# Kernel tuning notes

Measured on AMD Instinct MI355X. Metric: run time of the kernel, lower is better.

Reference implementation:

```python
import math
import jax, jax.numpy as jnp
import numpy as np

L, W, H, T, B = 12, 1024, 16, 1024, 2
CH = W // H  # per-head channels
SCALE = 1.0 / math.sqrt(math.sqrt(CH))
STD = 0.25 * math.sqrt(1.0 / W)  # init_scale * sqrt(1/width)


def setup_inputs() -> dict:
    key = jax.random.key(0)
    ks = jax.random.split(key, 8)
    x = jax.random.normal(ks[0], (B, T, W), dtype=jnp.float32)
    qkv_w = jax.random.normal(ks[1], (L, W, 3 * W), dtype=jnp.float32) * STD
    qkv_b = jnp.zeros((L, 3 * W), jnp.float32)
    proj_w = jax.random.normal(ks[2], (L, W, W), dtype=jnp.float32) * STD
    proj_b = jnp.zeros((L, W), jnp.float32)
    ln1_g = jnp.ones((L, W), jnp.float32)
    ln1_b = jnp.zeros((L, W), jnp.float32)
    ln2_g = jnp.ones((L, W), jnp.float32)
    ln2_b = jnp.zeros((L, W), jnp.float32)
    fc_w = jax.random.normal(ks[3], (L, W, 4 * W), dtype=jnp.float32) * STD
    fc_b = jnp.zeros((L, 4 * W), jnp.float32)
    fc2_w = jax.random.normal(ks[4], (L, 4 * W, W), dtype=jnp.float32) * STD
    fc2_b = jnp.zeros((L, W), jnp.float32)
    return dict(x=x, qkv_w=qkv_w, qkv_b=qkv_b, proj_w=proj_w, proj_b=proj_b,
                ln1_g=ln1_g, ln1_b=ln1_b, ln2_g=ln2_g, ln2_b=ln2_b,
                fc_w=fc_w, fc_b=fc_b, fc2_w=fc2_w, fc2_b=fc2_b)


def _ln(x, g, b, eps=1e-5):
    mu = jnp.mean(x, axis=-1, keepdims=True)
    var = jnp.mean(jnp.square(x - mu), axis=-1, keepdims=True)
    return (x - mu) * jax.lax.rsqrt(var + eps) * g + b


def _attn(h, w_qkv, b_qkv, w_p, b_p):
    bs, t, w = h.shape
    qkv = (h @ w_qkv + b_qkv).reshape(bs, t, H, 3 * CH)
    q, k, v = jnp.split(qkv, 3, axis=-1)  # each [bs, t, H, CH]
    # double-sqrt scaling as in QKVMultiheadAttention
    wts = jnp.einsum('bthc,bshc->bhts', q * SCALE, k * SCALE)
    wts = jax.nn.softmax(wts.astype(jnp.float32), axis=-1).astype(h.dtype)
    o = jnp.einsum('bhts,bshc->bthc', wts, v).reshape(bs, t, w)
    return o @ w_p + b_p


def reference(x, qkv_w, qkv_b, proj_w, proj_b, ln1_g, ln1_b, ln2_g, ln2_b,
              fc_w, fc_b, fc2_w, fc2_b):
    def step(h, p):
        wq, bq, wp, bp, g1, b1, g2, b2, wf, bf, w2, b2m = p
        h = h + _attn(_ln(h, g1, b1), wq, bq, wp, bp)
        z = _ln(h, g2, b2)
        h = h + (jax.nn.gelu(z @ wf + bf, approximate=False) @ w2 + b2m)
        return h, None
    params = (qkv_w, qkv_b, proj_w, proj_b, ln1_g, ln1_b, ln2_g, ln2_b,
              fc_w, fc_b, fc2_w, fc2_b)
    out, _ = jax.lax.scan(step, x, params)
    return out
```

## Files before the change

kernel.cpp:

```cpp
#include <hip/hip_runtime.h>
#include <hip/hip_bf16.h>
#include <math.h>

typedef __bf16 bf16;
typedef __bf16 bf16x8 __attribute__((ext_vector_type(8)));
typedef __bf16 bf16x4 __attribute__((ext_vector_type(4)));
typedef float  f32x4  __attribute__((ext_vector_type(4)));

#define DEV __device__ __forceinline__

DEV void lds_load16(const void* g, void* l) {
  __builtin_amdgcn_global_load_lds(
      (__attribute__((address_space(1))) unsigned int*)g,
      (__attribute__((address_space(3))) unsigned int*)l, 16, 0, 0);
}

DEV f32x4 mfma16(bf16x8 a, bf16x8 b, f32x4 c) {
  return __builtin_amdgcn_mfma_f32_16x16x32_bf16(a, b, c, 0, 0, 0);
}

__global__ void copy_f32(const float* __restrict__ in, float* __restrict__ out) {
  int i = blockIdx.x * blockDim.x + threadIdx.x;
  ((float4*)out)[i] = ((const float4*)in)[i];
}

__global__ __launch_bounds__(256) void transpose_cvt(
    const float* __restrict__ in0, bf16* __restrict__ out0, int R, int C) {
  __shared__ float t[32][33];
  size_t zo = (size_t)blockIdx.z * R * C;
  const float* in = in0 + zo;
  bf16* out = out0 + zo;
  int tx = threadIdx.x, ty = threadIdx.y;
  int c0 = blockIdx.x * 32, r0 = blockIdx.y * 32;
#pragma unroll
  for (int i = 0; i < 4; i++)
    t[ty + i * 8][tx] = in[(size_t)(r0 + ty + i * 8) * C + c0 + tx];
  __syncthreads();
#pragma unroll
  for (int i = 0; i < 4; i++)
    out[(size_t)(c0 + ty + i * 8) * R + r0 + tx] = (bf16)t[tx][ty + i * 8];
}

__global__ __launch_bounds__(256) void ln_fwd(
    const float* __restrict__ x, const float* __restrict__ gw,
    const float* __restrict__ bw, bf16* __restrict__ y) {
  int row = blockIdx.x, tid = threadIdx.x;
  const float4 v = ((const float4*)(x + (size_t)row * 1024))[tid];
  float s  = v.x + v.y + v.z + v.w;
  float s2 = v.x * v.x + v.y * v.y + v.z * v.z + v.w * v.w;
#pragma unroll
  for (int o = 1; o < 64; o <<= 1) {
    s  += __shfl_xor(s, o);
    s2 += __shfl_xor(s2, o);
  }
  __shared__ float ps[4], ps2[4];
  int wv = tid >> 6;
  if ((tid & 63) == 0) { ps[wv] = s; ps2[wv] = s2; }
  __syncthreads();
  s  = ps[0] + ps[1] + ps[2] + ps[3];
  s2 = ps2[0] + ps2[1] + ps2[2] + ps2[3];
  float mu  = s * (1.f / 1024.f);
  float var = s2 * (1.f / 1024.f) - mu * mu;
  float rs  = rsqrtf(var + 1e-5f);
  float4 gv = ((const float4*)gw)[tid];
  float4 bv = ((const float4*)bw)[tid];
  bf16x4 o4;
  o4[0] = (bf16)((v.x - mu) * rs * gv.x + bv.x);
  o4[1] = (bf16)((v.y - mu) * rs * gv.y + bv.y);
  o4[2] = (bf16)((v.z - mu) * rs * gv.z + bv.z);
  o4[3] = (bf16)((v.w - mu) * rs * gv.w + bv.w);
  *(bf16x4*)(y + (size_t)row * 1024 + tid * 4) = o4;
}

__global__ __launch_bounds__(256) void reduce_ln(
    const float* __restrict__ parts, int nparts, const float* __restrict__ bias,
    float* __restrict__ h, const float* __restrict__ gw,
    const float* __restrict__ bw, bf16* __restrict__ y) {
  const int row = blockIdx.x, tid = threadIdx.x;
  const size_t MN = (size_t)gridDim.x * 1024;
  const size_t rb = (size_t)row * 256;
  float4 s = ((const float4*)parts)[rb + tid];
  for (int p = 1; p < nparts; p++) {
    float4 v = ((const float4*)(parts + (size_t)p * MN))[rb + tid];
    s.x += v.x; s.y += v.y; s.z += v.z; s.w += v.w;
  }
  const float4 bb = ((const float4*)bias)[tid];
  float4 r = ((float4*)h)[rb + tid];
  r.x += s.x + bb.x; r.y += s.y + bb.y; r.z += s.z + bb.z; r.w += s.w + bb.w;
  ((float4*)h)[rb + tid] = r;
  if (gw == nullptr) return;
  float sm  = r.x + r.y + r.z + r.w;
  float sm2 = r.x * r.x + r.y * r.y + r.z * r.z + r.w * r.w;
#pragma unroll
  for (int o = 1; o < 64; o <<= 1) {
    sm  += __shfl_xor(sm, o);
    sm2 += __shfl_xor(sm2, o);
  }
  __shared__ float ps[4], ps2[4];
  int wv = tid >> 6;
  if ((tid & 63) == 0) { ps[wv] = sm; ps2[wv] = sm2; }
  __syncthreads();
  sm  = ps[0] + ps[1] + ps[2] + ps[3];
  sm2 = ps2[0] + ps2[1] + ps2[2] + ps2[3];
  float mu  = sm * (1.f / 1024.f);
  float var = sm2 * (1.f / 1024.f) - mu * mu;
  float rs  = rsqrtf(var + 1e-5f);
  float4 gv = ((const float4*)gw)[tid];
  float4 bv = ((const float4*)bw)[tid];
  bf16x4 o4;
  o4[0] = (bf16)((r.x - mu) * rs * gv.x + bv.x);
  o4[1] = (bf16)((r.y - mu) * rs * gv.y + bv.y);
  o4[2] = (bf16)((r.z - mu) * rs * gv.z + bv.z);
  o4[3] = (bf16)((r.w - mu) * rs * gv.w + bv.w);
  *(bf16x4*)(y + (size_t)row * 1024 + tid * 4) = o4;
}

template <int EPI>
__global__ __launch_bounds__(512, 2) void gemm8p(
    const bf16* __restrict__ A, const bf16* __restrict__ Bt,
    const float* __restrict__ bias, float* __restrict__ outf,
    bf16* __restrict__ outb, int M, int N, int K, int kcount) {
  __shared__ __align__(16) char lds[3 * 49152];
  const int tid = threadIdx.x, wv = tid >> 6, lane = tid & 63;
  const int g = lane >> 4, lr = lane & 15;
  const int wr = wv >> 2, wc = wv & 3;
  const int bn = blockIdx.x, bm = blockIdx.y;
  const int kbegin = blockIdx.z * kcount;
  const bf16* Ab = A + (size_t)bm * 128 * K + kbegin;
  const bf16* Bb = Bt + (size_t)bn * 256 * K + kbegin;
  const int nt = kcount >> 6;

  f32x4 acc[4][4] = {};

  auto stageA = [&](int t) {
    char* dst = lds + (t % 3) * 49152;
    int k0 = t * 64;
#pragma unroll
    for (int c = 0; c < 2; c++) {
      int off = c * 8192 + tid * 16;
      int row = off >> 7, cb = off & 127;
      int cbs = cb ^ ((row & 7) << 4);
      lds_load16((const char*)(Ab + (size_t)row * K + k0) + cbs, dst + off);
    }
  };
  auto stageB = [&](int t, int half) {
    char* dst = lds + (t % 3) * 49152 + 16384 + half * 16384;
    int k0 = t * 64;
#pragma unroll
    for (int c = 0; c < 2; c++) {
      int off = c * 8192 + tid * 16;
      int row = (off >> 7) + half * 128, cb = off & 127;
      int cbs = cb ^ ((row & 7) << 4);
      lds_load16((const char*)(Bb + (size_t)row * K + k0) + cbs, dst + off);
    }
  };
  auto ldA = [&](int t, int m, int kk) -> bf16x8 {
    const char* base = lds + (t % 3) * 49152;
    int row = wr * 64 + m * 16 + lr;
    int col = (kk * 64 + g * 16) ^ ((row & 7) << 4);
    return *(const bf16x8*)(base + row * 128 + col);
  };
  auto ldB = [&](int t, int n, int kk) -> bf16x8 {
    const char* base = lds + (t % 3) * 49152 + 16384;
    int row = wc * 64 + n * 16 + lr;
    int col = (kk * 64 + g * 16) ^ ((row & 7) << 4);
    return *(const bf16x8*)(base + row * 128 + col);
  };

  stageA(0); stageB(0, 0); stageB(0, 1);
  if (nt > 1) {
    stageA(1); stageB(1, 0); stageB(1, 1);
    asm volatile("s_waitcnt vmcnt(6)" ::: "memory");
  } else {
    asm volatile("s_waitcnt vmcnt(0)" ::: "memory");
  }
  __builtin_amdgcn_s_barrier();

  bf16x8 a[4][2], b[4][2];
  for (int t = 0; t < nt; ++t) {
#pragma unroll
    for (int m = 0; m < 4; m++)
#pragma unroll
      for (int kk = 0; kk < 2; kk++) a[m][kk] = ldA(t, m, kk);
#pragma unroll
    for (int n = 0; n < 2; n++)
#pragma unroll
      for (int kk = 0; kk < 2; kk++) b[n][kk] = ldB(t, n, kk);
    if (t + 2 < nt) { stageA(t + 2); stageB(t + 2, 0); }
    __builtin_amdgcn_s_barrier();
    asm volatile("s_waitcnt lgkmcnt(0)" ::: "memory");
    __builtin_amdgcn_sched_barrier(0);
    __builtin_amdgcn_s_setprio(1);
#pragma unroll
    for (int m = 0; m < 4; m++)
#pragma unroll
      for (int n = 0; n < 2; n++)
#pragma unroll
        for (int kk = 0; kk < 2; kk++)
          acc[m][n] = mfma16(a[m][kk], b[n][kk], acc[m][n]);
    __builtin_amdgcn_s_setprio(0);
    __builtin_amdgcn_s_barrier();
#pragma unroll
    for (int n = 2; n < 4; n++)
#pragma unroll
      for (int kk = 0; kk < 2; kk++) b[n][kk] = ldB(t, n, kk);
    if (t + 2 < nt) {
      stageB(t + 2, 1);
      asm volatile("s_waitcnt vmcnt(6)" ::: "memory");
    } else if (t + 1 < nt) {
      asm volatile("s_waitcnt vmcnt(0)" ::: "memory");
    }
    __builtin_amdgcn_s_barrier();
    asm volatile("s_waitcnt lgkmcnt(0)" ::: "memory");
    __builtin_amdgcn_sched_barrier(0);
    __builtin_amdgcn_s_setprio(1);
#pragma unroll
    for (int m = 0; m < 4; m++)
#pragma unroll
      for (int n = 2; n < 4; n++)
#pragma unroll
        for (int kk = 0; kk < 2; kk++)
          acc[m][n] = mfma16(a[m][kk], b[n][kk], acc[m][n]);
    __builtin_amdgcn_s_setprio(0);
    __builtin_amdgcn_s_barrier();
  }

  float* po = (EPI == 3) ? outf + (size_t)blockIdx.z * M * N : outf;
#pragma unroll
  for (int m = 0; m < 4; m++) {
#pragma unroll
    for (int n = 0; n < 4; n++) {
      int col = bn * 256 + wc * 64 + n * 16 + lr;
      float bv = (EPI == 3) ? 0.f : bias[col];
#pragma unroll
      for (int r = 0; r < 4; r++) {
        int row = bm * 128 + wr * 64 + m * 16 + g * 4 + r;
        size_t idx = (size_t)row * N + col;
        float v = acc[m][n][r] + bv;
        if (EPI == 0) {
          outb[idx] = (bf16)v;
        } else if (EPI == 2) {
          outb[idx] = (bf16)(0.5f * v * (1.f + erff(v * 0.70710678118f)));
        } else {
          po[idx] = v;
        }
      }
    }
  }
}

__global__ __launch_bounds__(256) void attn_fwd(
    const bf16* __restrict__ qkv, bf16* __restrict__ outp) {
  __shared__ __align__(16) bf16 Kls[128 * 64];
  __shared__ __align__(16) bf16 Vt[64 * 128];
  __shared__ __align__(16) bf16 Pls[4 * 32 * 128];
  const int tid = threadIdx.x, wv = tid >> 6, lane = tid & 63;
  const int g = lane >> 4, lr = lane & 15;
  const int bh = blockIdx.y, bb = bh >> 4, hh = bh & 15;
  const int q0 = blockIdx.x * 128;
  const bf16* base = qkv + (size_t)bb * 1024 * 3072;
  const int qc = hh * 192, kc = qc + 64, vc = qc + 128;

  bf16x8 aq[2][2];
#pragma unroll
  for (int m = 0; m < 2; m++)
#pragma unroll
    for (int kk = 0; kk < 2; kk++) {
      int row = q0 + wv * 32 + m * 16 + lr;
      aq[m][kk] = *(const bf16x8*)(base + (size_t)row * 3072 + qc + kk * 32 + g * 8);
    }

  f32x4 o[2][4] = {};
  float rm[2][4], rl[2][4];
#pragma unroll
  for (int m = 0; m < 2; m++)
#pragma unroll
    for (int r = 0; r < 4; r++) { rm[m][r] = -1e30f; rl[m][r] = 0.f; }

  for (int s0 = 0; s0 < 1024; s0 += 128) {
#pragma unroll
    for (int c = 0; c < 4; c++) {
      int off = wv * 4096 + c * 1024 + lane * 16;
      int s = off >> 7, cb = off & 127;
      int cbs = cb ^ ((s & 7) << 4);
      lds_load16((const char*)(base + (size_t)(s0 + s) * 3072 + kc) + cbs,
                 (char*)Kls + off);
    }
#pragma unroll
    for (int it = 0; it < 4; it++) {
      int idx = it * 256 + tid;
      int s = idx >> 3, c0i = (idx & 7) * 8;
      bf16x8 vvv = *(const bf16x8*)(base + (size_t)(s0 + s) * 3072 + vc + c0i);
#pragma unroll
      for (int j = 0; j < 8; j++) {
        int c = c0i + j;
        *(bf16*)((char*)Vt + c * 256 + ((s * 2) ^ ((c & 7) << 4))) = vvv[j];
      }
    }
    __syncthreads();
    f32x4 sa[2][8] = {};
#pragma unroll
    for (int kk = 0; kk < 2; kk++) {
#pragma unroll
      for (int n = 0; n < 8; n++) {
        int srow = n * 16 + lr;
        int cbyte = (kk * 32 + g * 8) * 2;
        bf16x8 kb = *(const bf16x8*)((char*)Kls + srow * 128 +
                                     (cbyte ^ ((srow & 7) << 4)));
        sa[0][n] = mfma16(aq[0][kk], kb, sa[0][n]);
        sa[1][n] = mfma16(aq[1][kk], kb, sa[1][n]);
      }
    }
#pragma unroll
    for (int m = 0; m < 2; m++) {
      float al[4];
#pragma unroll
      for (int r = 0; r < 4; r++) {
        float tm = -1e30f;
#pragma unroll
        for (int n = 0; n < 8; n++) {
          sa[m][n][r] *= 0.125f;
          tm = fmaxf(tm, sa[m][n][r]);
        }
        tm = fmaxf(tm, __shfl_xor(tm, 1));
        tm = fmaxf(tm, __shfl_xor(tm, 2));
        tm = fmaxf(tm, __shfl_xor(tm, 4));
        tm = fmaxf(tm, __shfl_xor(tm, 8));
        float nm = fmaxf(rm[m][r], tm);
        al[r] = __expf(rm[m][r] - nm);
        rm[m][r] = nm;
      }
      float psum[4] = {0.f, 0.f, 0.f, 0.f};
#pragma unroll
      for (int n = 0; n < 8; n++) {
#pragma unroll
        for (int r = 0; r < 4; r++) {
          float p = __expf(sa[m][n][r] - rm[m][r]);
          psum[r] += p;
          int rw = m * 16 + g * 4 + r;
          int sb = (n * 16 + lr) * 2;
          *(bf16*)((char*)Pls + wv * 8192 + rw * 256 + (sb ^ ((rw & 7) << 4))) =
              (bf16)p;
        }
      }
#pragma unroll
      for (int r = 0; r < 4; r++) {
        psum[r] += __shfl_xor(psum[r], 1);
        psum[r] += __shfl_xor(psum[r], 2);
        psum[r] += __shfl_xor(psum[r], 4);
        psum[r] += __shfl_xor(psum[r], 8);
        rl[m][r] = rl[m][r] * al[r] + psum[r];
#pragma unroll
        for (int n = 0; n < 4; n++) o[m][n][r] *= al[r];
      }
    }
    __syncthreads();
#pragma unroll
    for (int sc = 0; sc < 4; sc++) {
      bf16x8 pa[2];
#pragma unroll
      for (int m = 0; m < 2; m++) {
        int rw = m * 16 + lr;
        int sb = (sc * 32 + g * 8) * 2;
        pa[m] = *(const bf16x8*)((char*)Pls + wv * 8192 + rw * 256 +
                                 (sb ^ ((rw & 7) << 4)));
      }
#pragma unroll
      for (int n = 0; n < 4; n++) {
        int c = n * 16 + lr;
        int sb = (sc * 32 + g * 8) * 2;
        bf16x8 vb = *(const bf16x8*)((char*)Vt + c * 256 + (sb ^ ((c & 7) << 4)));
        o[0][n] = mfma16(pa[0], vb, o[0][n]);
        o[1][n] = mfma16(pa[1], vb, o[1][n]);
      }
    }
    __syncthreads();
  }
#pragma unroll
  for (int m = 0; m < 2; m++)
#pragma unroll
    for (int n = 0; n < 4; n++)
#pragma unroll
      for (int r = 0; r < 4; r++) {
        int row = q0 + wv * 32 + m * 16 + g * 4 + r;
        int col = hh * 64 + n * 16 + lr;
        outp[(size_t)(bb * 1024 + row) * 1024 + col] =
            (bf16)(o[m][n][r] / rl[m][r]);
      }
}

extern "C" void kernel_launch(void* const* d_in, const int* in_sizes, int n_in,
                              void* d_out, int out_size, void* d_ws,
                              size_t ws_size, hipStream_t stream) {
  const float* x      = (const float*)d_in[0];
  const float* qkv_w  = (const float*)d_in[1];
  const float* qkv_b  = (const float*)d_in[2];
  const float* proj_w = (const float*)d_in[3];
  const float* proj_b = (const float*)d_in[4];
  const float* ln1_g  = (const float*)d_in[5];
  const float* ln1_b  = (const float*)d_in[6];
  const float* ln2_g  = (const float*)d_in[7];
  const float* ln2_b  = (const float*)d_in[8];
  const float* fc_w   = (const float*)d_in[9];
  const float* fc_b   = (const float*)d_in[10];
  const float* fc2_w  = (const float*)d_in[11];
  const float* fc2_b  = (const float*)d_in[12];
  float* h = (float*)d_out;

  char* ws = (char*)d_ws;
  size_t off = 0;
  auto alloc = [&](size_t bytes) -> char* {
    char* p = ws + off;
    off = (off + bytes + 255) & ~(size_t)255;
    return p;
  };
  bf16* wq_t    = (bf16*)alloc((size_t)12 * 3072 * 1024 * 2);
  bf16* wp_t    = (bf16*)alloc((size_t)12 * 1024 * 1024 * 2);
  bf16* wf_t    = (bf16*)alloc((size_t)12 * 4096 * 1024 * 2);
  bf16* w2_t    = (bf16*)alloc((size_t)12 * 1024 * 4096 * 2);
  bf16* lnbuf   = (bf16*)alloc((size_t)2048 * 1024 * 2);
  bf16* qkvbuf  = (bf16*)alloc((size_t)2048 * 3072 * 2);
  bf16* attnbuf = (bf16*)alloc((size_t)2048 * 1024 * 2);
  bf16* fcbuf   = (bf16*)alloc((size_t)2048 * 4096 * 2);
  float* partbuf = (float*)alloc((size_t)4 * 2048 * 1024 * 4);

  transpose_cvt<<<dim3(96, 32, 12), dim3(32, 8), 0, stream>>>(qkv_w, wq_t, 1024, 3072);
  transpose_cvt<<<dim3(32, 32, 12), dim3(32, 8), 0, stream>>>(proj_w, wp_t, 1024, 1024);
  transpose_cvt<<<dim3(128, 32, 12), dim3(32, 8), 0, stream>>>(fc_w, wf_t, 1024, 4096);
  transpose_cvt<<<dim3(32, 128, 12), dim3(32, 8), 0, stream>>>(fc2_w, w2_t, 4096, 1024);

  copy_f32<<<2048, 256, 0, stream>>>(x, h);
  ln_fwd<<<2048, 256, 0, stream>>>(h, ln1_g, ln1_b, lnbuf);

  for (int l = 0; l < 12; l++) {
    const bf16* wq = wq_t + (size_t)l * 3072 * 1024;
    const bf16* wp = wp_t + (size_t)l * 1024 * 1024;
    const bf16* wf = wf_t + (size_t)l * 4096 * 1024;
    const bf16* w2 = w2_t + (size_t)l * 1024 * 4096;

    gemm8p<0><<<dim3(12, 16, 1), 512, 0, stream>>>(
        lnbuf, wq, qkv_b + (size_t)l * 3072, nullptr, qkvbuf, 2048, 3072, 1024,
        1024);
    attn_fwd<<<dim3(8, 32), 256, 0, stream>>>(qkvbuf, attnbuf);
    gemm8p<3><<<dim3(4, 16, 2), 512, 0, stream>>>(
        attnbuf, wp, nullptr, partbuf, nullptr, 2048, 1024, 1024, 512);
    reduce_ln<<<2048, 256, 0, stream>>>(partbuf, 2, proj_b + (size_t)l * 1024,
                                        h, ln2_g + (size_t)l * 1024,
                                        ln2_b + (size_t)l * 1024, lnbuf);
    gemm8p<2><<<dim3(16, 16, 1), 512, 0, stream>>>(
        lnbuf, wf, fc_b + (size_t)l * 4096, nullptr, fcbuf, 2048, 4096, 1024,
        1024);
    gemm8p<3><<<dim3(4, 16, 4), 512, 0, stream>>>(
        fcbuf, w2, nullptr, partbuf, nullptr, 2048, 1024, 4096, 1024);
    if (l < 11) {
      reduce_ln<<<2048, 256, 0, stream>>>(
          partbuf, 4, fc2_b + (size_t)l * 1024, h,
          ln1_g + (size_t)(l + 1) * 1024, ln1_b + (size_t)(l + 1) * 1024,
          lnbuf);
    } else {
      reduce_ln<<<2048, 256, 0, stream>>>(partbuf, 4,
                                          fc2_b + (size_t)l * 1024, h, nullptr,
                                          nullptr, nullptr);
    }
  }
}
```

Measured before the change: 2.035 ms.

## Load GEMM A operand straight to registers, stage only B in LDS

The GEMM now reads the A tile directly from global memory into registers for each k-step and uses LDS only for the B tile. This frees LDS, allowing a 128-wide N tile for the projection and FC2 GEMMs. FC2 split-K drops from 4 to 2, which halves the partial buffer and the reduce traffic. The initial copy kernel is folded into the first layernorm. The direct A loads lose LDS reuse across the four column waves, so more global/L2 traffic is exchanged for lower LDS pressure and fewer barriers.

```diff
diff --git a/kernel.cpp b/kernel.cpp
--- a/kernel.cpp
+++ b/kernel.cpp
@@ -17,11 +17,6 @@
 
 DEV f32x4 mfma16(bf16x8 a, bf16x8 b, f32x4 c) {
   return __builtin_amdgcn_mfma_f32_16x16x32_bf16(a, b, c, 0, 0, 0);
-}
-
-__global__ void copy_f32(const float* __restrict__ in, float* __restrict__ out) {
-  int i = blockIdx.x * blockDim.x + threadIdx.x;
-  ((float4*)out)[i] = ((const float4*)in)[i];
 }
 
 __global__ __launch_bounds__(256) void transpose_cvt(
@@ -43,9 +38,11 @@
 
 __global__ __launch_bounds__(256) void ln_fwd(
     const float* __restrict__ x, const float* __restrict__ gw,
-    const float* __restrict__ bw, bf16* __restrict__ y) {
+    const float* __restrict__ bw, bf16* __restrict__ y,
+    float* __restrict__ hout) {
   int row = blockIdx.x, tid = threadIdx.x;
   const float4 v = ((const float4*)(x + (size_t)row * 1024))[tid];
+  if (hout) ((float4*)(hout + (size_t)row * 1024))[tid] = v;
   float s  = v.x + v.y + v.z + v.w;
   float s2 = v.x * v.x + v.y * v.y + v.z * v.z + v.w * v.w;
 #pragma unroll
@@ -115,122 +112,128 @@
   *(bf16x4*)(y + (size_t)row * 1024 + tid * 4) = o4;
 }
 
-template <int EPI>
-__global__ __launch_bounds__(512, 2) void gemm8p(
+template <int BN, int EPI>
+__global__ __launch_bounds__(512, 2) void gemm_ad(
     const bf16* __restrict__ A, const bf16* __restrict__ Bt,
     const float* __restrict__ bias, float* __restrict__ outf,
     bf16* __restrict__ outb, int M, int N, int K, int kcount) {
-  __shared__ __align__(16) char lds[3 * 49152];
+  constexpr int NF = BN / 64;
+  constexpr int SLOT = BN * 64 * 2;
+  constexpr int NCH = BN / 64;
+  __shared__ __align__(16) char lds[3 * SLOT];
   const int tid = threadIdx.x, wv = tid >> 6, lane = tid & 63;
   const int g = lane >> 4, lr = lane & 15;
   const int wr = wv >> 2, wc = wv & 3;
   const int bn = blockIdx.x, bm = blockIdx.y;
   const int kbegin = blockIdx.z * kcount;
-  const bf16* Ab = A + (size_t)bm * 128 * K + kbegin;
-  const bf16* Bb = Bt + (size_t)bn * 256 * K + kbegin;
+  const bf16* Ab =
+      A + (size_t)(bm * 128 + wr * 64 + lr) * K + kbegin + g * 8;
+  const bf16* Bb = Bt + (size_t)bn * BN * K + kbegin;
   const int nt = kcount >> 6;
-
-  f32x4 acc[4][4] = {};
-
-  auto stageA = [&](int t) {
-    char* dst = lds + (t % 3) * 49152;
-    int k0 = t * 64;
-#pragma unroll
-    for (int c = 0; c < 2; c++) {
-      int off = c * 8192 + tid * 16;
-      int row = off >> 7, cb = off & 127;
-      int cbs = cb ^ ((row & 7) << 4);
-      lds_load16((const char*)(Ab + (size_t)row * K + k0) + cbs, dst + off);
-    }
+  f32x4 acc[4][NF] = {};
+
+  auto stageC = [&](int t, int c) {
+    char* dst = lds + (t % 3) * SLOT;
+    int off = c * 8192 + tid * 16;
+    int row = off >> 7, cb = off & 127;
+    lds_load16((const char*)(Bb + (size_t)row * K + t * 64) +
+                   (cb ^ ((row & 7) << 4)),
+               dst + off);
   };
-  auto stageB = [&](int t, int half) {
-    char* dst = lds + (t % 3) * 49152 + 16384 + half * 16384;
-    int k0 = t * 64;
-#pragma unroll
-    for (int c = 0; c < 2; c++) {
-      int off = c * 8192 + tid * 16;
-      int row = (off >> 7) + half * 128, cb = off & 127;
-      int cbs = cb ^ ((row & 7) << 4);
-      lds_load16((const char*)(Bb + (size_t)row * K + k0) + cbs, dst + off);
-    }
-  };
-  auto ldA = [&](int t, int m, int kk) -> bf16x8 {
-    const char* base = lds + (t % 3) * 49152;
-    int row = wr * 64 + m * 16 + lr;
+  auto ldB = [&](int t, int n, int kk) -> bf16x8 {
+    const char* base = lds + (t % 3) * SLOT;
+    int row = wc * (BN / 4) + n * 16 + lr;
     int col = (kk * 64 + g * 16) ^ ((row & 7) << 4);
     return *(const bf16x8*)(base + row * 128 + col);
   };
-  auto ldB = [&](int t, int n, int kk) -> bf16x8 {
-    const char* base = lds + (t % 3) * 49152 + 16384;
-    int row = wc * 64 + n * 16 + lr;
-    int col = (kk * 64 + g * 16) ^ ((row & 7) << 4);
-    return *(const bf16x8*)(base + row * 128 + col);
-  };
-
-  stageA(0); stageB(0, 0); stageB(0, 1);
-  if (nt > 1) {
-    stageA(1); stageB(1, 0); stageB(1, 1);
-    asm volatile("s_waitcnt vmcnt(6)" ::: "memory");
-  } else {
-    asm volatile("s_waitcnt vmcnt(0)" ::: "memory");
-  }
+
+  for (int c = 0; c < NCH; c++) stageC(0, c);
+  if (nt > 1)
+    for (int c = 0; c < NCH; c++) stageC(1, c);
+  if (NCH == 4)
+    asm volatile("s_waitcnt vmcnt(4)" ::: "memory");
+  else
+    asm volatile("s_waitcnt vmcnt(2)" ::: "memory");
   __builtin_amdgcn_s_barrier();
 
-  bf16x8 a[4][2], b[4][2];
   for (int t = 0; t < nt; ++t) {
+    bf16x8 a[4][2];
 #pragma unroll
     for (int m = 0; m < 4; m++)
 #pragma unroll
-      for (int kk = 0; kk < 2; kk++) a[m][kk] = ldA(t, m, kk);
-#pragma unroll
-    for (int n = 0; n < 2; n++)
-#pragma unroll
-      for (int kk = 0; kk < 2; kk++) b[n][kk] = ldB(t, n, kk);
-    if (t + 2 < nt) { stageA(t + 2); stageB(t + 2, 0); }
-    __builtin_amdgcn_s_barrier();
-    asm volatile("s_waitcnt lgkmcnt(0)" ::: "memory");
-    __builtin_amdgcn_sched_barrier(0);
-    __builtin_amdgcn_s_setprio(1);
-#pragma unroll
-    for (int m = 0; m < 4; m++)
+      for (int kk = 0; kk < 2; kk++)
+        a[m][kk] =
+            *(const bf16x8*)(Ab + (size_t)m * 16 * K + t * 64 + kk * 32);
+
+    if constexpr (BN == 256) {
+      bf16x8 b[2][2];
 #pragma unroll
       for (int n = 0; n < 2; n++)
 #pragma unroll
-        for (int kk = 0; kk < 2; kk++)
-          acc[m][n] = mfma16(a[m][kk], b[n][kk], acc[m][n]);
-    __builtin_amdgcn_s_setprio(0);
-    __builtin_amdgcn_s_barrier();
-#pragma unroll
-    for (int n = 2; n < 4; n++)
-#pragma unroll
-      for (int kk = 0; kk < 2; kk++) b[n][kk] = ldB(t, n, kk);
-    if (t + 2 < nt) {
-      stageB(t + 2, 1);
-      asm volatile("s_waitcnt vmcnt(6)" ::: "memory");
-    } else if (t + 1 < nt) {
-      asm volatile("s_waitcnt vmcnt(0)" ::: "memory");
-    }
-    __builtin_amdgcn_s_barrier();
-    asm volatile("s_waitcnt lgkmcnt(0)" ::: "memory");
-    __builtin_amdgcn_sched_barrier(0);
-    __builtin_amdgcn_s_setprio(1);
-#pragma unroll
-    for (int m = 0; m < 4; m++)
-#pragma unroll
-      for (int n = 2; n < 4; n++)
-#pragma unroll
-        for (int kk = 0; kk < 2; kk++)
-          acc[m][n] = mfma16(a[m][kk], b[n][kk], acc[m][n]);
-    __builtin_amdgcn_s_setprio(0);
-    __builtin_amdgcn_s_barrier();
+        for (int kk = 0; kk < 2; kk++) b[n][kk] = ldB(t, n, kk);
+      if (t + 2 < nt) { stageC(t + 2, 0); stageC(t + 2, 1); }
+      __builtin_amdgcn_s_barrier();
+      asm volatile("s_waitcnt lgkmcnt(0)" ::: "memory");
+      __builtin_amdgcn_sched_barrier(0);
+      __builtin_amdgcn_s_setprio(1);
+#pragma unroll
+      for (int m = 0; m < 4; m++)
+#pragma unroll
+        for (int n = 0; n < 2; n++)
+#pragma unroll
+          for (int kk = 0; kk < 2; kk++)
+            acc[m][n] = mfma16(a[m][kk], b[n][kk], acc[m][n]);
+      __builtin_amdgcn_s_setprio(0);
+      __builtin_amdgcn_s_barrier();
+#pragma unroll
+      for (int n = 0; n < 2; n++)
+#pragma unroll
+        for (int kk = 0; kk < 2; kk++) b[n][kk] = ldB(t, n + 2, kk);
+      if (t + 2 < nt) { stageC(t + 2, 2); stageC(t + 2, 3); }
+      asm volatile("s_waitcnt vmcnt(4)" ::: "memory");
+      __builtin_amdgcn_s_barrier();
+      asm volatile("s_waitcnt lgkmcnt(0)" ::: "memory");
+      __builtin_amdgcn_sched_barrier(0);
+      __builtin_amdgcn_s_setprio(1);
+#pragma unroll
+      for (int m = 0; m < 4; m++)
+#pragma unroll
+        for (int n = 0; n < 2; n++)
+#pragma unroll
+          for (int kk = 0; kk < 2; kk++)
+            acc[m][n + 2] = mfma16(a[m][kk], b[n][kk], acc[m][n + 2]);
+      __builtin_amdgcn_s_setprio(0);
+      __builtin_amdgcn_s_barrier();
+    } else {
+      bf16x8 b[NF][2];
+#pragma unroll
+      for (int n = 0; n < NF; n++)
+#pragma unroll
+        for (int kk = 0; kk < 2; kk++) b[n][kk] = ldB(t, n, kk);
+      if (t + 2 < nt) { stageC(t + 2, 0); stageC(t + 2, 1); }
+      asm volatile("s_waitcnt vmcnt(2)" ::: "memory");
+      __builtin_amdgcn_s_barrier();
+      asm volatile("s_waitcnt lgkmcnt(0)" ::: "memory");
+      __builtin_amdgcn_sched_barrier(0);
+      __builtin_amdgcn_s_setprio(1);
+#pragma unroll
+      for (int m = 0; m < 4; m++)
+#pragma unroll
+        for (int n = 0; n < NF; n++)
+#pragma unroll
+          for (int kk = 0; kk < 2; kk++)
+            acc[m][n] = mfma16(a[m][kk], b[n][kk], acc[m][n]);
+      __builtin_amdgcn_s_setprio(0);
+      __builtin_amdgcn_s_barrier();
+    }
   }
 
   float* po = (EPI == 3) ? outf + (size_t)blockIdx.z * M * N : outf;
 #pragma unroll
   for (int m = 0; m < 4; m++) {
 #pragma unroll
-    for (int n = 0; n < 4; n++) {
-      int col = bn * 256 + wc * 64 + n * 16 + lr;
+    for (int n = 0; n < NF; n++) {
+      int col = bn * BN + wc * (BN / 4) + n * 16 + lr;
       float bv = (EPI == 3) ? 0.f : bias[col];
 #pragma unroll
       for (int r = 0; r < 4; r++) {
@@ -422,15 +425,14 @@
   bf16* qkvbuf  = (bf16*)alloc((size_t)2048 * 3072 * 2);
   bf16* attnbuf = (bf16*)alloc((size_t)2048 * 1024 * 2);
   bf16* fcbuf   = (bf16*)alloc((size_t)2048 * 4096 * 2);
-  float* partbuf = (float*)alloc((size_t)4 * 2048 * 1024 * 4);
+  float* partbuf = (float*)alloc((size_t)2 * 2048 * 1024 * 4);
 
   transpose_cvt<<<dim3(96, 32, 12), dim3(32, 8), 0, stream>>>(qkv_w, wq_t, 1024, 3072);
   transpose_cvt<<<dim3(32, 32, 12), dim3(32, 8), 0, stream>>>(proj_w, wp_t, 1024, 1024);
   transpose_cvt<<<dim3(128, 32, 12), dim3(32, 8), 0, stream>>>(fc_w, wf_t, 1024, 4096);
   transpose_cvt<<<dim3(32, 128, 12), dim3(32, 8), 0, stream>>>(fc2_w, w2_t, 4096, 1024);
 
-  copy_f32<<<2048, 256, 0, stream>>>(x, h);
-  ln_fwd<<<2048, 256, 0, stream>>>(h, ln1_g, ln1_b, lnbuf);
+  ln_fwd<<<2048, 256, 0, stream>>>(x, ln1_g, ln1_b, lnbuf, h);
 
   for (int l = 0; l < 12; l++) {
     const bf16* wq = wq_t + (size_t)l * 3072 * 1024;
@@ -438,27 +440,27 @@
     const bf16* wf = wf_t + (size_t)l * 4096 * 1024;
     const bf16* w2 = w2_t + (size_t)l * 1024 * 4096;
 
-    gemm8p<0><<<dim3(12, 16, 1), 512, 0, stream>>>(
+    gemm_ad<256, 0><<<dim3(12, 16, 1), 512, 0, stream>>>(
         lnbuf, wq, qkv_b + (size_t)l * 3072, nullptr, qkvbuf, 2048, 3072, 1024,
         1024);
     attn_fwd<<<dim3(8, 32), 256, 0, stream>>>(qkvbuf, attnbuf);
-    gemm8p<3><<<dim3(4, 16, 2), 512, 0, stream>>>(
+    gemm_ad<128, 3><<<dim3(8, 16, 2), 512, 0, stream>>>(
         attnbuf, wp, nullptr, partbuf, nullptr, 2048, 1024, 1024, 512);
     reduce_ln<<<2048, 256, 0, stream>>>(partbuf, 2, proj_b + (size_t)l * 1024,
                                         h, ln2_g + (size_t)l * 1024,
                                         ln2_b + (size_t)l * 1024, lnbuf);
-    gemm8p<2><<<dim3(16, 16, 1), 512, 0, stream>>>(
+    gemm_ad<256, 2><<<dim3(16, 16, 1), 512, 0, stream>>>(
         lnbuf, wf, fc_b + (size_t)l * 4096, nullptr, fcbuf, 2048, 4096, 1024,
         1024);
-    gemm8p<3><<<dim3(4, 16, 4), 512, 0, stream>>>(
-        fcbuf, w2, nullptr, partbuf, nullptr, 2048, 1024, 4096, 1024);
+    gemm_ad<128, 3><<<dim3(8, 16, 2), 512, 0, stream>>>(
+        fcbuf, w2, nullptr, partbuf, nullptr, 2048, 1024, 4096, 2048);
     if (l < 11) {
       reduce_ln<<<2048, 256, 0, stream>>>(
-          partbuf, 4, fc2_b + (size_t)l * 1024, h,
+          partbuf, 2, fc2_b + (size_t)l * 1024, h,
           ln1_g + (size_t)(l + 1) * 1024, ln1_b + (size_t)(l + 1) * 1024,
           lnbuf);
     } else {
-      reduce_ln<<<2048, 256, 0, stream>>>(partbuf, 4,
+      reduce_ln<<<2048, 256, 0, stream>>>(partbuf, 2,
                                           fc2_b + (size_t)l * 1024, h, nullptr,
                                           nullptr, nullptr);
     }
```

Measured after the change: 3.604 ms. 1.77x slower.

## Halve attention query tile to double grid, fold scale into Q, use exp2

Applied to the files above, without the earlier changes.

The attention kernel now gives each block 64 query rows (16 per wave) instead of 128, so the grid doubles from 256 to 512 blocks and fills more compute units, at the cost of reloading K/V tiles twice as often. The softmax scale and log2(e) are folded into Q when it is loaded, so the softmax can use exp2f without a per-score multiply. V transposition into LDS now packs two rows per 32-bit store. The separate copy kernel is removed by having the first layernorm also write the residual buffer.

```diff
diff --git a/kernel.cpp b/kernel.cpp
--- a/kernel.cpp
+++ b/kernel.cpp
@@ -17,11 +17,6 @@
 
 DEV f32x4 mfma16(bf16x8 a, bf16x8 b, f32x4 c) {
   return __builtin_amdgcn_mfma_f32_16x16x32_bf16(a, b, c, 0, 0, 0);
-}
-
-__global__ void copy_f32(const float* __restrict__ in, float* __restrict__ out) {
-  int i = blockIdx.x * blockDim.x + threadIdx.x;
-  ((float4*)out)[i] = ((const float4*)in)[i];
 }
 
 __global__ __launch_bounds__(256) void transpose_cvt(
@@ -43,9 +38,11 @@
 
 __global__ __launch_bounds__(256) void ln_fwd(
     const float* __restrict__ x, const float* __restrict__ gw,
-    const float* __restrict__ bw, bf16* __restrict__ y) {
+    const float* __restrict__ bw, bf16* __restrict__ y,
+    float* __restrict__ hout) {
   int row = blockIdx.x, tid = threadIdx.x;
   const float4 v = ((const float4*)(x + (size_t)row * 1024))[tid];
+  if (hout) ((float4*)(hout + (size_t)row * 1024))[tid] = v;
   float s  = v.x + v.y + v.z + v.w;
   float s2 = v.x * v.x + v.y * v.y + v.z * v.z + v.w * v.w;
 #pragma unroll
@@ -253,29 +250,30 @@
     const bf16* __restrict__ qkv, bf16* __restrict__ outp) {
   __shared__ __align__(16) bf16 Kls[128 * 64];
   __shared__ __align__(16) bf16 Vt[64 * 128];
-  __shared__ __align__(16) bf16 Pls[4 * 32 * 128];
+  __shared__ __align__(16) bf16 Pls[4 * 16 * 128];
   const int tid = threadIdx.x, wv = tid >> 6, lane = tid & 63;
   const int g = lane >> 4, lr = lane & 15;
   const int bh = blockIdx.y, bb = bh >> 4, hh = bh & 15;
-  const int q0 = blockIdx.x * 128;
+  const int q0 = blockIdx.x * 64;
   const bf16* base = qkv + (size_t)bb * 1024 * 3072;
   const int qc = hh * 192, kc = qc + 64, vc = qc + 128;
 
-  bf16x8 aq[2][2];
-#pragma unroll
-  for (int m = 0; m < 2; m++)
+  bf16x8 aq[2];
+  {
+    int row = q0 + wv * 16 + lr;
 #pragma unroll
     for (int kk = 0; kk < 2; kk++) {
-      int row = q0 + wv * 32 + m * 16 + lr;
-      aq[m][kk] = *(const bf16x8*)(base + (size_t)row * 3072 + qc + kk * 32 + g * 8);
-    }
-
-  f32x4 o[2][4] = {};
-  float rm[2][4], rl[2][4];
-#pragma unroll
-  for (int m = 0; m < 2; m++)
-#pragma unroll
-    for (int r = 0; r < 4; r++) { rm[m][r] = -1e30f; rl[m][r] = 0.f; }
+      bf16x8 v = *(const bf16x8*)(base + (size_t)row * 3072 + qc + kk * 32 + g * 8);
+#pragma unroll
+      for (int j = 0; j < 8; j++) v[j] = (bf16)((float)v[j] * 0.1803368801f);
+      aq[kk] = v;
+    }
+  }
+
+  f32x4 o[4] = {};
+  float rm[4], rl[4];
+#pragma unroll
+  for (int r = 0; r < 4; r++) { rm[r] = -1e30f; rl[r] = 0.f; }
 
   for (int s0 = 0; s0 < 1024; s0 += 128) {
 #pragma unroll
@@ -287,18 +285,21 @@
                  (char*)Kls + off);
     }
 #pragma unroll
-    for (int it = 0; it < 4; it++) {
+    for (int it = 0; it < 2; it++) {
       int idx = it * 256 + tid;
-      int s = idx >> 3, c0i = (idx & 7) * 8;
-      bf16x8 vvv = *(const bf16x8*)(base + (size_t)(s0 + s) * 3072 + vc + c0i);
+      int s = (idx >> 3) * 2, c0i = (idx & 7) * 8;
+      bf16x8 v0 = *(const bf16x8*)(base + (size_t)(s0 + s) * 3072 + vc + c0i);
+      bf16x8 v1 = *(const bf16x8*)(base + (size_t)(s0 + s + 1) * 3072 + vc + c0i);
 #pragma unroll
       for (int j = 0; j < 8; j++) {
         int c = c0i + j;
-        *(bf16*)((char*)Vt + c * 256 + ((s * 2) ^ ((c & 7) << 4))) = vvv[j];
+        unsigned int pk = (unsigned int)__builtin_bit_cast(unsigned short, v0[j]) |
+                          ((unsigned int)__builtin_bit_cast(unsigned short, v1[j]) << 16);
+        *(unsigned int*)((char*)Vt + c * 256 + ((s * 2) ^ ((c & 7) << 4))) = pk;
       }
     }
     __syncthreads();
-    f32x4 sa[2][8] = {};
+    f32x4 sa[8] = {};
 #pragma unroll
     for (int kk = 0; kk < 2; kk++) {
 #pragma unroll
@@ -307,86 +308,69 @@
         int cbyte = (kk * 32 + g * 8) * 2;
         bf16x8 kb = *(const bf16x8*)((char*)Kls + srow * 128 +
                                      (cbyte ^ ((srow & 7) << 4)));
-        sa[0][n] = mfma16(aq[0][kk], kb, sa[0][n]);
-        sa[1][n] = mfma16(aq[1][kk], kb, sa[1][n]);
+        sa[n] = mfma16(aq[kk], kb, sa[n]);
       }
     }
-#pragma unroll
-    for (int m = 0; m < 2; m++) {
-      float al[4];
+    float al[4];
+#pragma unroll
+    for (int r = 0; r < 4; r++) {
+      float tm = -1e30f;
+#pragma unroll
+      for (int n = 0; n < 8; n++) tm = fmaxf(tm, sa[n][r]);
+      tm = fmaxf(tm, __shfl_xor(tm, 1));
+      tm = fmaxf(tm, __shfl_xor(tm, 2));
+      tm = fmaxf(tm, __shfl_xor(tm, 4));
+      tm = fmaxf(tm, __shfl_xor(tm, 8));
+      float nm = fmaxf(rm[r], tm);
+      al[r] = exp2f(rm[r] - nm);
+      rm[r] = nm;
+    }
+    float psum[4] = {0.f, 0.f, 0.f, 0.f};
+#pragma unroll
+    for (int n = 0; n < 8; n++) {
 #pragma unroll
       for (int r = 0; r < 4; r++) {
-        float tm = -1e30f;
-#pragma unroll
-        for (int n = 0; n < 8; n++) {
-          sa[m][n][r] *= 0.125f;
-          tm = fmaxf(tm, sa[m][n][r]);
-        }
-        tm = fmaxf(tm, __shfl_xor(tm, 1));
-        tm = fmaxf(tm, __shfl_xor(tm, 2));
-        tm = fmaxf(tm, __shfl_xor(tm, 4));
-        tm = fmaxf(tm, __shfl_xor(tm, 8));
-        float nm = fmaxf(rm[m][r], tm);
-        al[r] = __expf(rm[m][r] - nm);
-        rm[m][r] = nm;
+        float p = exp2f(sa[n][r] - rm[r]);
+        psum[r] += p;
+        int rw = g * 4 + r;
+        int sb = (n * 16 + lr) * 2;
+        *(bf16*)((char*)Pls + wv * 4096 + rw * 256 + (sb ^ ((rw & 7) << 4))) =
+            (bf16)p;
       }
-      float psum[4] = {0.f, 0.f, 0.f, 0.f};
-#pragma unroll
-      for (int n = 0; n < 8; n++) {
-#pragma unroll
-        for (int r = 0; r < 4; r++) {
-          float p = __expf(sa[m][n][r] - rm[m][r]);
-          psum[r] += p;
-          int rw = m * 16 + g * 4 + r;
-          int sb = (n * 16 + lr) * 2;
-          *(bf16*)((char*)Pls + wv * 8192 + rw * 256 + (sb ^ ((rw & 7) << 4))) =
-              (bf16)p;
-        }
-      }
-#pragma unroll
-      for (int r = 0; r < 4; r++) {
-        psum[r] += __shfl_xor(psum[r], 1);
-        psum[r] += __shfl_xor(psum[r], 2);
-        psum[r] += __shfl_xor(psum[r], 4);
-        psum[r] += __shfl_xor(psum[r], 8);
-        rl[m][r] = rl[m][r] * al[r] + psum[r];
-#pragma unroll
-        for (int n = 0; n < 4; n++) o[m][n][r] *= al[r];
-      }
+    }
+#pragma unroll
+    for (int r = 0; r < 4; r++) {
+      psum[r] += __shfl_xor(psum[r], 1);
+      psum[r] += __shfl_xor(psum[r], 2);
+      psum[r] += __shfl_xor(psum[r], 4);
+      psum[r] += __shfl_xor(psum[r], 8);
+      rl[r] = rl[r] * al[r] + psum[r];
+#pragma unroll
+      for (int n = 0; n < 4; n++) o[n][r] *= al[r];
     }
     __syncthreads();
 #pragma unroll
     for (int sc = 0; sc < 4; sc++) {
-      bf16x8 pa[2];
-#pragma unroll
-      for (int m = 0; m < 2; m++) {
-        int rw = m * 16 + lr;
-        int sb = (sc * 32 + g * 8) * 2;
-        pa[m] = *(const bf16x8*)((char*)Pls + wv * 8192 + rw * 256 +
-                                 (sb ^ ((rw & 7) << 4)));
-      }
+      int sb = (sc * 32 + g * 8) * 2;
+      bf16x8 pa = *(const bf16x8*)((char*)Pls + wv * 4096 + lr * 256 +
+                                   (sb ^ ((lr & 7) << 4)));
 #pragma unroll
       for (int n = 0; n < 4; n++) {
         int c = n * 16 + lr;
-        int sb = (sc * 32 + g * 8) * 2;
         bf16x8 vb = *(const bf16x8*)((char*)Vt + c * 256 + (sb ^ ((c & 7) << 4)));
-        o[0][n] = mfma16(pa[0], vb, o[0][n]);
-        o[1][n] = mfma16(pa[1], vb, o[1][n]);
+        o[n] = mfma16(pa, vb, o[n]);
       }
     }
     __syncthreads();
   }
 #pragma unroll
-  for (int m = 0; m < 2; m++)
-#pragma unroll
-    for (int n = 0; n < 4; n++)
-#pragma unroll
-      for (int r = 0; r < 4; r++) {
-        int row = q0 + wv * 32 + m * 16 + g * 4 + r;
-        int col = hh * 64 + n * 16 + lr;
-        outp[(size_t)(bb * 1024 + row) * 1024 + col] =
-            (bf16)(o[m][n][r] / rl[m][r]);
-      }
+  for (int n = 0; n < 4; n++)
+#pragma unroll
+    for (int r = 0; r < 4; r++) {
+      int row = q0 + wv * 16 + g * 4 + r;
+      int col = hh * 64 + n * 16 + lr;
+      outp[(size_t)(bb * 1024 + row) * 1024 + col] = (bf16)(o[n][r] / rl[r]);
+    }
 }
 
 extern "C" void kernel_launch(void* const* d_in, const int* in_sizes, int n_in,
@@ -429,8 +413,7 @@
   transpose_cvt<<<dim3(128, 32, 12), dim3(32, 8), 0, stream>>>(fc_w, wf_t, 1024, 4096);
   transpose_cvt<<<dim3(32, 128, 12), dim3(32, 8), 0, stream>>>(fc2_w, w2_t, 4096, 1024);
 
-  copy_f32<<<2048, 256, 0, stream>>>(x, h);
-  ln_fwd<<<2048, 256, 0, stream>>>(h, ln1_g, ln1_b, lnbuf);
+  ln_fwd<<<2048, 256, 0, stream>>>(x, ln1_g, ln1_b, lnbuf, h);
 
   for (int l = 0; l < 12; l++) {
     const bf16* wq = wq_t + (size_t)l * 3072 * 1024;
@@ -441,7 +424,7 @@
     gemm8p<0><<<dim3(12, 16, 1), 512, 0, stream>>>(
         lnbuf, wq, qkv_b + (size_t)l * 3072, nullptr, qkvbuf, 2048, 3072, 1024,
         1024);
-    attn_fwd<<<dim3(8, 32), 256, 0, stream>>>(qkvbuf, attnbuf);
+    attn_fwd<<<dim3(16, 32), 256, 0, stream>>>(qkvbuf, attnbuf);
     gemm8p<3><<<dim3(4, 16, 2), 512, 0, stream>>>(
         attnbuf, wp, nullptr, partbuf, nullptr, 2048, 1024, 1024, 512);
     reduce_ln<<<2048, 256, 0, stream>>>(partbuf, 2, proj_b + (size_t)l * 1024,
```

New measurement: 1.884 ms. -7.5%, faster.
